# Performance work log

Hardware: AMD Instinct MI355X
Metric: run time of the kernel (lower is better)

Reference implementation:

```python
import jax, jax.numpy as jnp
import numpy as np

_C0 = 0.28209479177387814
_C1 = 0.4886025119029199
_C2 = (1.0925484305920792, -1.0925484305920792, 0.31539156525252005, -1.0925484305920792, 0.5462742152960396)
_C3 = (-0.5900435899266435, 2.890611442640554, -0.4570457994644658, 0.3731763325901154, -0.4570457994644658, 1.445305721320277, -0.5900435899266435)

NEAR_PLANE = 0.8
FAR_PLANE = 1000.0
ALPHA_SKIP = 1.0 / 255.0
ALPHA_CLAMP = 0.99
ACC_BREAK = 0.9999


def _quat_to_rotmat(q):
    # q = (x, y, z, w), already normalized. Returns [N,3,3].
    x, y, z, w = q[:, 0], q[:, 1], q[:, 2], q[:, 3]
    r = jnp.stack([
        1 - 2 * (y * y + z * z), 2 * (x * y - z * w), 2 * (x * z + y * w),
        2 * (x * y + z * w), 1 - 2 * (x * x + z * z), 2 * (y * z - x * w),
        2 * (x * z - y * w), 2 * (y * z + x * w), 1 - 2 * (x * x + y * y)], axis=-1)
    return r.reshape(-1, 3, 3)


def _sh_basis(d):
    # d: [..., 3] unit directions -> [..., 16] degree-3 real SH basis.
    x, y, z = d[..., 0], d[..., 1], d[..., 2]
    xx, yy, zz = x * x, y * y, z * z
    return jnp.stack([
        jnp.full_like(x, _C0),
        -_C1 * y, _C1 * z, -_C1 * x,
        _C2[0] * x * y, _C2[1] * y * z, _C2[2] * (2 * zz - xx - yy), _C2[3] * x * z, _C2[4] * (xx - yy),
        _C3[0] * y * (3 * xx - yy), _C3[1] * x * y * z, _C3[2] * y * (4 * zz - xx - yy),
        _C3[3] * z * (2 * zz - 3 * xx - 3 * yy), _C3[4] * x * (4 * zz - xx - yy),
        _C3[5] * z * (xx - yy), _C3[6] * x * (xx - 3 * yy)], axis=-1)


def setup_inputs() -> dict:
    key = jax.random.key(0)
    k1, k2, k3, k4, k5, k6, k7 = jax.random.split(key, 7)
    N = 256
    H = W = 256
    fx = fy = 200.0
    cx, cy = W / 2.0, H / 2.0
    # Sample pixel locations + depths, back-project so points lie in the frustum.
    u = jax.random.uniform(k1, (N,), minval=8.0, maxval=W - 8.0)
    v = jax.random.uniform(k2, (N,), minval=8.0, maxval=H - 8.0)
    z = jax.random.uniform(k3, (N,), minval=2.0, maxval=10.0)
    pointcloud = jnp.stack([(u - cx) * z / fx, (v - cy) * z / fy, z], axis=-1).astype(jnp.float32)
    q = jax.random.normal(k4, (N, 4))
    log_s = jax.random.normal(k5, (N, 3)) * 0.3 - 1.5  # exp() -> world scale ~0.1-0.4
    alpha = jax.random.normal(k6, (N, 1)) + 1.0        # sigmoid -> mostly opaque-ish
    sh = jax.random.normal(k7, (N, 48)) * 0.3
    pointcloud_features = jnp.concatenate([q, log_s, alpha, sh], axis=-1).astype(jnp.float32)
    camera_intrinsics = jnp.array([[fx, 0.0, cx], [0.0, fy, cy], [0.0, 0.0, 1.0]], dtype=jnp.float32)
    T_camera_pointcloud = jnp.eye(4, dtype=jnp.float32)
    return {"pointcloud": pointcloud, "pointcloud_features": pointcloud_features,
            "camera_intrinsics": camera_intrinsics, "T_camera_pointcloud": T_camera_pointcloud,
            "camera_height": H, "camera_width": W}


def _rasterize(pointcloud, feats, K, T, H, W):
    R, t = T[:3, :3], T[:3, 3]
    p_cam = pointcloud @ R.T + t                      # [N,3] camera-frame points
    zc = p_cam[:, 2]
    proj = p_cam @ K.T
    uv = proj[:, :2] / jnp.clip(zc, 1e-6)[:, None]    # [N,2] pixel means
    in_cam = ((zc > NEAR_PLANE) & (zc < FAR_PLANE) &
              (uv[:, 0] >= 0) & (uv[:, 0] < W) & (uv[:, 1] >= 0) & (uv[:, 1] < H))
    # Global front-to-back depth sort (culled points pushed to the end).
    order = jnp.argsort(jnp.where(in_cam, zc, jnp.float32(1e10)))
    feats, uv, p_cam, zc, in_cam = feats[order], uv[order], p_cam[order], zc[order], in_cam[order]
    # 3D covariance = R(q) diag(exp(s))^2 R(q)^T
    q = feats[:, :4]
    q = q / jnp.linalg.norm(q, axis=-1, keepdims=True)
    Rq = _quat_to_rotmat(q)                           # [N,3,3]
    s = jnp.exp(feats[:, 4:7])
    M = Rq * s[:, None, :]
    Sigma = M @ jnp.swapaxes(M, -1, -2)               # [N,3,3]
    # Projection Jacobian -> 2D covariance
    fx, fy = K[0, 0], K[1, 1]
    zero = jnp.zeros_like(zc)
    J = jnp.stack([jnp.stack([fx / zc, zero, -fx * p_cam[:, 0] / (zc * zc)], -1),
                   jnp.stack([zero, fy / zc, -fy * p_cam[:, 1] / (zc * zc)], -1)], axis=-2)  # [N,2,3]
    JW = J @ R
    cov = JW @ Sigma @ jnp.swapaxes(JW, -1, -2)       # [N,2,2]
    det = jnp.maximum(cov[:, 0, 0] * cov[:, 1, 1] - cov[:, 0, 1] * cov[:, 1, 0], 1e-12)
    ia, ib, ic = cov[:, 1, 1] / det, -cov[:, 0, 1] / det, cov[:, 0, 0] / det
    # Per-pixel Gaussian density at pixel centers (u+0.5, v+0.5)
    px = jnp.arange(W, dtype=jnp.float32) + 0.5
    py = jnp.arange(H, dtype=jnp.float32) + 0.5
    dx = uv[:, 0, None] - px[None, :]                 # [N,W]
    dy = uv[:, 1, None] - py[None, :]                 # [N,H]
    quad = (ia[:, None, None] * (dx * dx)[:, None, :]
            + ic[:, None, None] * (dy * dy)[:, :, None]
            + 2.0 * ib[:, None, None] * dy[:, :, None] * dx[:, None, :])  # [N,H,W]
    gauss = jnp.exp(-0.5 * quad) / (2.0 * jnp.pi * jnp.sqrt(det))[:, None, None]
    a = gauss * jax.nn.sigmoid(feats[:, 7])[:, None, None]
    a = jnp.where(a < ALPHA_SKIP, 0.0, jnp.minimum(a, ALPHA_CLAMP))
    a = jnp.where(in_cam[:, None, None], a, 0.0)
    # Sequential compositing in closed form: acc is a running SUM of alphas,
    # point i is composited iff cumsum up to and including i stays <= 0.9999
    # (matches the 'break' in the Taichi kernel since skipped points have a=0).
    C = jnp.cumsum(a, axis=0)
    include = (C <= ACC_BREAK).astype(a.dtype)
    wgt = a * (1.0 - (C - a)) * include               # alpha_i * (1 - acc_before_i)
    # Per-pixel view directions in world frame for SH color
    Kinv = jnp.linalg.inv(K)
    u_grid, v_grid = jnp.meshgrid(jnp.arange(W, dtype=jnp.float32), jnp.arange(H, dtype=jnp.float32))
    pix = jnp.stack([u_grid, v_grid, jnp.ones_like(u_grid)], axis=-1)  # [H,W,3]
    d_world = (pix @ Kinv.T) @ R                      # R_wc = R^T applied to camera-frame dir
    d_world = d_world / jnp.linalg.norm(d_world, axis=-1, keepdims=True)
    sh = _sh_basis(d_world)                           # [H,W,16]
    coeffs = feats[:, 8:56].reshape(-1, 3, 16)        # [N,3,16] rgb SH coefficients
    color = jax.nn.sigmoid(jnp.einsum('hwk,nck->nhwc', sh, coeffs))
    image = jnp.einsum('nhw,nhwc->hwc', wgt, color)   # [H,W,3]
    return image


def reference(pointcloud, pointcloud_features, camera_intrinsics, T_camera_pointcloud, camera_height, camera_width):
    return _rasterize(pointcloud, pointcloud_features, camera_intrinsics,
                      T_camera_pointcloud, camera_height, camera_width)
```

## Files before the change

### kernel.cpp

```cpp
#include <hip/hip_runtime.h>
#include <math.h>
#include <float.h>

#define NEAR_PLANE 0.8f
#define FAR_PLANE 1000.0f
#define ALPHA_SKIP (1.0f/255.0f)
#define ALPHA_CLAMP 0.99f
#define ACC_BREAK 0.9999f

__global__ __launch_bounds__(256)
void fused_raster(const float* __restrict__ pts,
                  const float* __restrict__ feats,
                  const float* __restrict__ K,
                  const float* __restrict__ T,
                  const int* __restrict__ Hp,
                  const int* __restrict__ Wp,
                  float* __restrict__ out,
                  int N) {
    __shared__ unsigned long long s_mask[4];
    __shared__ float c_key[256];
    __shared__ int   c_id[256];
    __shared__ float4 r_p0[256];
    __shared__ float4 r_p1[256];

    const int t  = threadIdx.x;
    const int Wd = *Wp, Hd = *Hp;
    const int tilesX = (Wd + 15) >> 4;
    const int tilesY = (Hd + 15) >> 4;
    if ((int)blockIdx.x >= tilesX * tilesY) return;
    const int tileX = blockIdx.x % tilesX;
    const int tileY = blockIdx.x / tilesX;

    const float R00 = T[0],  R01 = T[1],  R02 = T[2],  ttx = T[3];
    const float R10 = T[4],  R11 = T[5],  R12 = T[6],  tty = T[7];
    const float R20 = T[8],  R21 = T[9],  R22 = T[10], ttz = T[11];

    float key = FLT_MAX;
    float pu = 0.f, pv = 0.f;
    float ia = 0.f, ib = 0.f, ic = 0.f, den = 1.f, sig = 0.f;
    bool cover = false;
    if (t < N) {
        const float px = pts[3*t], py = pts[3*t+1], pz = pts[3*t+2];
        const float* f = feats + 56*t;
        const float4 fq = *(const float4*)f;
        const float4 fs = *(const float4*)(f + 4);

        const float cxv = R00*px + R01*py + R02*pz + ttx;
        const float cyv = R10*px + R11*py + R12*pz + tty;
        const float czv = R20*px + R21*py + R22*pz + ttz;
        const float zc = czv;
        const float denom = fmaxf(zc, 1e-6f);
        const float K00 = K[0], K01 = K[1], K02 = K[2];
        const float K10 = K[3], K11 = K[4], K12 = K[5];
        pu = (K00*cxv + K01*cyv + K02*czv) / denom;
        pv = (K10*cxv + K11*cyv + K12*czv) / denom;
        const bool in_cam = (zc > NEAR_PLANE) && (zc < FAR_PLANE) &&
                            (pu >= 0.0f) && (pu < (float)Wd) &&
                            (pv >= 0.0f) && (pv < (float)Hd);
        key = in_cam ? zc : 1e10f;

        if (in_cam) {
            float qx = fq.x, qy = fq.y, qz = fq.z, qw = fq.w;
            const float qn = sqrtf(qx*qx + qy*qy + qz*qz + qw*qw);
            qx /= qn; qy /= qn; qz /= qn; qw /= qn;
            const float Q00 = 1.0f - 2.0f*(qy*qy + qz*qz);
            const float Q01 = 2.0f*(qx*qy - qz*qw);
            const float Q02 = 2.0f*(qx*qz + qy*qw);
            const float Q10 = 2.0f*(qx*qy + qz*qw);
            const float Q11 = 1.0f - 2.0f*(qx*qx + qz*qz);
            const float Q12 = 2.0f*(qy*qz - qx*qw);
            const float Q20 = 2.0f*(qx*qz - qy*qw);
            const float Q21 = 2.0f*(qy*qz + qx*qw);
            const float Q22 = 1.0f - 2.0f*(qx*qx + qy*qy);
            const float s0 = expf(fs.x), s1 = expf(fs.y), s2 = expf(fs.z);
            const float M00 = Q00*s0, M01 = Q01*s1, M02 = Q02*s2;
            const float M10 = Q10*s0, M11 = Q11*s1, M12 = Q12*s2;
            const float M20 = Q20*s0, M21 = Q21*s1, M22 = Q22*s2;
            const float S00 = M00*M00 + M01*M01 + M02*M02;
            const float S01 = M00*M10 + M01*M11 + M02*M12;
            const float S02 = M00*M20 + M01*M21 + M02*M22;
            const float S11 = M10*M10 + M11*M11 + M12*M12;
            const float S12 = M10*M20 + M11*M21 + M12*M22;
            const float S22 = M20*M20 + M21*M21 + M22*M22;

            const float fx = K00, fy = K11;
            const float J00 = fx / czv;
            const float J02 = -fx * cxv / (czv * czv);
            const float J11 = fy / czv;
            const float J12 = -fy * cyv / (czv * czv);
            const float W00 = J00*R00 + J02*R20;
            const float W01 = J00*R01 + J02*R21;
            const float W02 = J00*R02 + J02*R22;
            const float W10 = J11*R10 + J12*R20;
            const float W11 = J11*R11 + J12*R21;
            const float W12 = J11*R12 + J12*R22;
            const float A00 = W00*S00 + W01*S01 + W02*S02;
            const float A01 = W00*S01 + W01*S11 + W02*S12;
            const float A02 = W00*S02 + W01*S12 + W02*S22;
            const float A10 = W10*S00 + W11*S01 + W12*S02;
            const float A11 = W10*S01 + W11*S11 + W12*S12;
            const float A12 = W10*S02 + W11*S12 + W12*S22;
            const float c00 = A00*W00 + A01*W01 + A02*W02;
            const float c01 = A00*W10 + A01*W11 + A02*W12;
            const float c10 = A10*W00 + A11*W01 + A12*W02;
            const float c11 = A10*W10 + A11*W11 + A12*W12;
            const float det = fmaxf(c00*c11 - c01*c10, 1e-12f);
            ia = c11 / det;
            ib = -c01 / det;
            ic = c00 / det;
            den = 2.0f * (float)M_PI * sqrtf(det);
            sig = 1.0f / (1.0f + expf(-fs.w));

            const float L = 2.0f * logf(sig * 255.0f / den);
            if (L > 0.0f) {
                const float qm = L + 0.02f;
                const float detc = ia*ic - ib*ib;
                int wlo = 0, whi = Wd - 1, hlo = 0, hhi = Hd - 1;
                if (detc > 0.0f) {
                    const float dxm = fminf(sqrtf(qm * ic / detc), 1.0e6f) + 1.0f;
                    const float dym = fminf(sqrtf(qm * ia / detc), 1.0e6f) + 1.0f;
                    wlo = max(0,      (int)floorf(pu - dxm - 0.5f));
                    whi = min(Wd - 1, (int)ceilf (pu + dxm - 0.5f));
                    hlo = max(0,      (int)floorf(pv - dym - 0.5f));
                    hhi = min(Hd - 1, (int)ceilf (pv + dym - 0.5f));
                }
                if (wlo <= whi && hlo <= hhi) {
                    const int tx0 = wlo >> 4, tx1 = whi >> 4;
                    const int ty0 = hlo >> 4, ty1 = hhi >> 4;
                    cover = (tileX >= tx0) && (tileX <= tx1) &&
                            (tileY >= ty0) && (tileY <= ty1);
                }
            }
        }
    }

    const unsigned long long bb = __ballot(cover);
    if ((t & 63) == 0) s_mask[t >> 6] = bb;
    __syncthreads();

    const int wi = t >> 6;
    const int lane = t & 63;
    int Kc = 0, base = 0;
    #pragma unroll
    for (int w = 0; w < 4; ++w) {
        const int pc = __popcll(s_mask[w]);
        if (w < wi) base += pc;
        Kc += pc;
    }

    const int wpx = tileX * 16 + (t & 15);
    const int hpx = tileY * 16 + (t >> 4);
    const bool valid = (wpx < Wd) && (hpx < Hd);
    float* o = out + 3 * (hpx * Wd + wpx);

    if (Kc == 0) {
        if (valid) { o[0] = 0.0f; o[1] = 0.0f; o[2] = 0.0f; }
        return;
    }

    const int p = base + __popcll(bb & ((1ULL << lane) - 1ULL));
    if (cover) { c_key[p] = key; c_id[p] = t; }
    __syncthreads();

    if (cover) {
        int rank = 0;
        for (int j = 0; j < Kc; ++j) {
            const float kj = c_key[j];
            rank += (int)((kj < key) || (kj == key && c_id[j] < t));
        }
        r_p0[rank] = make_float4(pu, pv, ia, ib);
        r_p1[rank] = make_float4(ic, den, sig, __int_as_float(t));
    }
    __syncthreads();

    const float uw = (float)wpx, vh = (float)hpx;
    {
    }
    const float k00 = K[0], k01 = K[1], k02 = K[2];
    const float k10 = K[3], k11 = K[4], k12 = K[5];
    const float k20 = K[6], k21 = K[7], k22 = K[8];
    const float d0 = k11*k22 - k12*k21;
    const float d1 = k12*k20 - k10*k22;
    const float d2 = k10*k21 - k11*k20;
    const float rdetK = 1.0f / (k00*d0 + k01*d1 + k02*d2);
    const float i00 = d0*rdetK, i01 = (k02*k21 - k01*k22)*rdetK, i02 = (k01*k12 - k02*k11)*rdetK;
    const float i10 = d1*rdetK, i11 = (k00*k22 - k02*k20)*rdetK, i12 = (k02*k10 - k00*k12)*rdetK;
    const float i20 = d2*rdetK, i21 = (k01*k20 - k00*k21)*rdetK, i22 = (k00*k11 - k01*k10)*rdetK;
    const float cx0 = i00*uw + i01*vh + i02;
    const float cy0 = i10*uw + i11*vh + i12;
    const float cz0 = i20*uw + i21*vh + i22;
    const float ddx = R00*cx0 + R10*cy0 + R20*cz0;
    const float ddy = R01*cx0 + R11*cy0 + R21*cz0;
    const float ddz = R02*cx0 + R12*cy0 + R22*cz0;
    const float rn = 1.0f / sqrtf(ddx*ddx + ddy*ddy + ddz*ddz);
    const float x = ddx*rn, y = ddy*rn, z = ddz*rn;
    const float xx = x*x, yy = y*y, zz = z*z;

    float sh[16];
    sh[0]  = 0.28209479177387814f;
    sh[1]  = -0.4886025119029199f * y;
    sh[2]  = 0.4886025119029199f * z;
    sh[3]  = -0.4886025119029199f * x;
    sh[4]  = 1.0925484305920792f * x * y;
    sh[5]  = -1.0925484305920792f * y * z;
    sh[6]  = 0.31539156525252005f * (2.0f*zz - xx - yy);
    sh[7]  = -1.0925484305920792f * x * z;
    sh[8]  = 0.5462742152960396f * (xx - yy);
    sh[9]  = -0.5900435899266435f * y * (3.0f*xx - yy);
    sh[10] = 2.890611442640554f * x * y * z;
    sh[11] = -0.4570457994644658f * y * (4.0f*zz - xx - yy);
    sh[12] = 0.3731763325901154f * z * (2.0f*zz - 3.0f*xx - 3.0f*yy);
    sh[13] = -0.4570457994644658f * x * (4.0f*zz - xx - yy);
    sh[14] = 1.445305721320277f * z * (xx - yy);
    sh[15] = -0.5900435899266435f * x * (xx - 3.0f*yy);

    const float pxc = uw + 0.5f;
    const float pyc = vh + 0.5f;
    float C = 0.0f;
    float img0 = 0.0f, img1 = 0.0f, img2 = 0.0f;

    for (int n = 0; n < Kc; ++n) {
        const float4 P0 = r_p0[n];
        const float4 P1 = r_p1[n];
        const float dx = P0.x - pxc;
        const float dy = P0.y - pyc;
        const float quad = P0.z*dx*dx + P1.x*dy*dy + 2.0f*P0.w*dy*dx;
        const float g = expf(-0.5f * quad) / P1.y;
        float a = g * P1.z;
        a = (a < ALPHA_SKIP) ? 0.0f : fminf(a, ALPHA_CLAMP);
        C += a;
        if (a > 0.0f && C <= ACC_BREAK) {
            const float wgt = a * (1.0f - (C - a));
            const float* cf = feats + 56*__float_as_int(P1.w) + 8;
            float t0 = 0.0f, t1 = 0.0f, t2 = 0.0f;
            #pragma unroll
            for (int kk = 0; kk < 16; ++kk) {
                const float bsh = sh[kk];
                t0 += bsh * cf[kk];
                t1 += bsh * cf[16 + kk];
                t2 += bsh * cf[32 + kk];
            }
            img0 += wgt * (1.0f / (1.0f + expf(-t0)));
            img1 += wgt * (1.0f / (1.0f + expf(-t1)));
            img2 += wgt * (1.0f / (1.0f + expf(-t2)));
        }
    }

    if (valid) {
        o[0] = img0;
        o[1] = img1;
        o[2] = img2;
    }
}

extern "C" void kernel_launch(void* const* d_in, const int* in_sizes, int n_in,
                              void* d_out, int out_size, void* d_ws, size_t ws_size,
                              hipStream_t stream) {
    const float* pts   = (const float*)d_in[0];
    const float* feats = (const float*)d_in[1];
    const float* K     = (const float*)d_in[2];
    const float* T     = (const float*)d_in[3];
    const int*   Hp    = (const int*)d_in[4];
    const int*   Wp    = (const int*)d_in[5];
    float* out = (float*)d_out;

    const int N = in_sizes[0] / 3;
    const int npix = out_size / 3;
    const int blocks = (npix + 255) / 256;

    fused_raster<<<blocks, 256, 0, stream>>>(pts, feats, K, T, Hp, Wp, out, N);
}
```

Before: 11.07 us.

## Stage sorted splat SH coefficients in shared memory and hoist global loads

The block now cooperatively copies the 48 SH coefficients of each depth-sorted covering splat into a 48KB shared buffer. The per-pixel compositing loop then reads coefficients from LDS instead of doing scattered global loads. The first chunk of the copy is issued before the SH basis math so its latency overlaps that work. The point and feature loads are also hoisted above the tile bounds check. The cost is much more shared memory per block, which may lower occupancy, plus an extra barrier.

```diff
diff --git a/kernel.cpp b/kernel.cpp
--- a/kernel.cpp
+++ b/kernel.cpp
@@ -22,8 +22,24 @@
     __shared__ int   c_id[256];
     __shared__ float4 r_p0[256];
     __shared__ float4 r_p1[256];
-
-    const int t  = threadIdx.x;
+    __shared__ float4 s_coef4[256*12];
+
+    const int t = threadIdx.x;
+
+    float px = 0.f, py = 0.f, pz = 0.f;
+    float4 fq = make_float4(0.f, 0.f, 0.f, 1.f);
+    float4 fs = make_float4(0.f, 0.f, 0.f, 0.f);
+    if (t < N) {
+        px = pts[3*t]; py = pts[3*t+1]; pz = pts[3*t+2];
+        const float* f = feats + 56*t;
+        fq = *(const float4*)f;
+        fs = *(const float4*)(f + 4);
+    }
+
+    const float R00 = T[0],  R01 = T[1],  R02 = T[2],  ttx = T[3];
+    const float R10 = T[4],  R11 = T[5],  R12 = T[6],  tty = T[7];
+    const float R20 = T[8],  R21 = T[9],  R22 = T[10], ttz = T[11];
+
     const int Wd = *Wp, Hd = *Hp;
     const int tilesX = (Wd + 15) >> 4;
     const int tilesY = (Hd + 15) >> 4;
@@ -31,20 +47,11 @@
     const int tileX = blockIdx.x % tilesX;
     const int tileY = blockIdx.x / tilesX;
 
-    const float R00 = T[0],  R01 = T[1],  R02 = T[2],  ttx = T[3];
-    const float R10 = T[4],  R11 = T[5],  R12 = T[6],  tty = T[7];
-    const float R20 = T[8],  R21 = T[9],  R22 = T[10], ttz = T[11];
-
     float key = FLT_MAX;
     float pu = 0.f, pv = 0.f;
     float ia = 0.f, ib = 0.f, ic = 0.f, den = 1.f, sig = 0.f;
     bool cover = false;
     if (t < N) {
-        const float px = pts[3*t], py = pts[3*t+1], pz = pts[3*t+2];
-        const float* f = feats + 56*t;
-        const float4 fq = *(const float4*)f;
-        const float4 fs = *(const float4*)(f + 4);
-
         const float cxv = R00*px + R01*py + R02*pz + ttx;
         const float cyv = R10*px + R11*py + R12*pz + tty;
         const float czv = R20*px + R21*py + R22*pz + ttz;
@@ -173,9 +180,16 @@
     }
     __syncthreads();
 
+    const int nElem = Kc * 12;
+    float4 v0;
+    int g0 = -1, q0 = 0;
+    if (t < nElem) {
+        g0 = t / 12; q0 = t - 12*g0;
+        const int gid = __float_as_int(r_p1[g0].w);
+        v0 = *(const float4*)(feats + 56*gid + 8 + 4*q0);
+    }
+
     const float uw = (float)wpx, vh = (float)hpx;
-    {
-    }
     const float k00 = K[0], k01 = K[1], k02 = K[2];
     const float k10 = K[3], k11 = K[4], k12 = K[5];
     const float k20 = K[6], k21 = K[7], k22 = K[8];
@@ -214,6 +228,15 @@
     sh[14] = 1.445305721320277f * z * (xx - yy);
     sh[15] = -0.5900435899266435f * x * (xx - 3.0f*yy);
 
+    if (g0 >= 0) s_coef4[12*g0 + q0] = v0;
+    for (int i = 256 + t; i < nElem; i += 256) {
+        const int g = i / 12, q = i - 12*g;
+        const int gid = __float_as_int(r_p1[g].w);
+        s_coef4[12*g + q] = *(const float4*)(feats + 56*gid + 8 + 4*q);
+    }
+    __syncthreads();
+
+    const float* s_coef = (const float*)s_coef4;
     const float pxc = uw + 0.5f;
     const float pyc = vh + 0.5f;
     float C = 0.0f;
@@ -231,7 +254,7 @@
         C += a;
         if (a > 0.0f && C <= ACC_BREAK) {
             const float wgt = a * (1.0f - (C - a));
-            const float* cf = feats + 56*__float_as_int(P1.w) + 8;
+            const float* cf = s_coef + 48*n;
             float t0 = 0.0f, t1 = 0.0f, t2 = 0.0f;
             #pragma unroll
             for (int kk = 0; kk < 16; ++kk) {
```

Measured after the change: 10.98 us. About the same (-0.7%).
